# Kernel optimization log

Hardware: AMD Instinct MI355X
Metric: run time of the kernel (lower is better)

## Reference

```python
import jax, jax.numpy as jnp
import numpy as np

EPS = 1e-5

def _layernorm(x, gamma, beta, axes):
    mean = jnp.mean(x, axis=axes, keepdims=True)
    var = jnp.var(x, axis=axes, keepdims=True)
    return (x - mean) * jax.lax.rsqrt(var + EPS) * gamma + beta

def setup_inputs() -> dict:
    key = jax.random.key(0)
    ks = jax.random.split(key, 14)
    B, N1, N2, D1, D2 = 128, 32, 32, 23, 13
    E, H, F = 72, 256, 128
    N = N1 + N2
    s = 0.05
    return {
        "x_a": jax.random.normal(ks[0], (B, N1, D1), jnp.float32),
        "x_b": jax.random.normal(ks[1], (B, N2, D2), jnp.float32),
        "W_a": jax.random.normal(ks[2], (D1, E), jnp.float32) * s,
        "b_a": jnp.zeros((E,), jnp.float32),
        "W_b": jax.random.normal(ks[3], (D2, E), jnp.float32) * s,
        "b_b": jnp.zeros((E,), jnp.float32),
        "ln0_g": jnp.ones((N, E), jnp.float32),
        "ln0_b": jnp.zeros((N, E), jnp.float32),
        "W_g": jax.random.normal(ks[4], (2 * E, H), jnp.float32) * s,
        "b_g": jnp.zeros((H,), jnp.float32),
        "lng_g": jnp.ones((H,), jnp.float32),
        "lng_b": jnp.zeros((H,), jnp.float32),
        "W_f": jax.random.normal(ks[5], (H, F), jnp.float32) * s,
        "b_f": jnp.zeros((F,), jnp.float32),
    }

def reference(x_a, x_b, W_a, b_a, W_b, b_b, ln0_g, ln0_b,
              W_g, b_g, lng_g, lng_b, W_f, b_f):
    # SplitEmbedding: per-group linear embed, concat along entity dim
    a = jnp.concatenate([x_a @ W_a + b_a, x_b @ W_b + b_b], axis=-2)  # [B, N, E]
    # LayerNorm over last two dims (num_entities, embed_dim) jointly
    a = _layernorm(a, ln0_g, ln0_b, axes=(-2, -1))
    B, N, E = a.shape
    # ij(): aij[b, i, j] = concat(a[b, i], a[b, j])  -> [B, N, N, 2E]
    ai = jnp.broadcast_to(a[:, :, None, :], (B, N, N, E))
    aj = jnp.broadcast_to(a[:, None, :, :], (B, N, N, E))
    aij = jnp.concatenate([ai, aj], axis=-1)
    # g: Linear(2E, H) + ELU, then LayerNorm(H)
    g = jax.nn.elu(aij @ W_g + b_g)  # [B, N, N, H]
    g = _layernorm(g, lng_g, lng_b, axes=(-1,))
    # sum over both pairwise dims
    s = jnp.sum(g, axis=(-3, -2))  # [B, H]
    # f: Linear(H, F) + ELU
    return jax.nn.elu(s @ W_f + b_f)  # [B, F]
```

## Files before the change

### kernel.cpp

```cpp
#include <hip/hip_runtime.h>
#include <hip/hip_bf16.h>

#define EPS 1e-5f

#define OFF_ABAR 0
#define OFF_U    589824
#define OFF_V    2686976
#define OFF_PART 4784128

__device__ __forceinline__ float elu(float z) {
    return z > 0.f ? z : __expf(z) - 1.f;
}

__global__ __launch_bounds__(256) void k_embed_ln0(
    const float* __restrict__ xa, const float* __restrict__ xb,
    const float* __restrict__ Wa, const float* __restrict__ ba,
    const float* __restrict__ Wb, const float* __restrict__ bb,
    const float* __restrict__ g0, const float* __restrict__ b0,
    float* __restrict__ abar) {
    int b = blockIdx.x;
    int tid = threadIdx.x;
    float vals[18];
    float s1 = 0.f, s2 = 0.f;
    for (int m = 0; m < 18; ++m) {
        int k = tid + 256 * m;
        int e = k % 72;
        int n = k / 72;
        float acc;
        if (n < 32) {
            acc = ba[e];
            const float* x = xa + (b * 32 + n) * 23;
            #pragma unroll
            for (int d = 0; d < 23; ++d) acc = fmaf(x[d], Wa[d * 72 + e], acc);
        } else {
            acc = bb[e];
            const float* x = xb + (b * 32 + (n - 32)) * 13;
            #pragma unroll
            for (int d = 0; d < 13; ++d) acc = fmaf(x[d], Wb[d * 72 + e], acc);
        }
        vals[m] = acc;
        s1 += acc;
        s2 = fmaf(acc, acc, s2);
    }
    #pragma unroll
    for (int off = 32; off >= 1; off >>= 1) {
        s1 += __shfl_xor(s1, off, 64);
        s2 += __shfl_xor(s2, off, 64);
    }
    __shared__ float r1[4], r2[4];
    int w = tid >> 6;
    if ((tid & 63) == 0) { r1[w] = s1; r2[w] = s2; }
    __syncthreads();
    float t1 = r1[0] + r1[1] + r1[2] + r1[3];
    float t2 = r2[0] + r2[1] + r2[2] + r2[3];
    float mean = t1 * (1.f / 4608.f);
    float var  = fmaf(-mean, mean, t2 * (1.f / 4608.f));
    float rsq  = rsqrtf(var + EPS);
    float* ab = abar + b * 4608;
    for (int m = 0; m < 18; ++m) {
        int k = tid + 256 * m;
        ab[k] = fmaf((vals[m] - mean) * rsq, g0[k], b0[k]);
    }
}

__global__ __launch_bounds__(256) void k_uv(
    const float* __restrict__ abar, const float* __restrict__ Wg,
    const float* __restrict__ bg,
    float* __restrict__ U, float* __restrict__ V) {
    int blk = blockIdx.x;
    int b = blk >> 2;
    int q = blk & 3;
    int h = threadIdx.x;
    __shared__ float sa[72 * 16];
    const float* src = abar + (b * 64 + q * 16) * 72;
    for (int k = threadIdx.x; k < 72 * 16; k += 256) {
        int e = k >> 4, n = k & 15;
        sa[k] = src[n * 72 + e];
    }
    __syncthreads();
    float u[16], v[16];
    #pragma unroll
    for (int n = 0; n < 16; ++n) { u[n] = 0.f; v[n] = 0.f; }
    for (int e = 0; e < 72; ++e) {
        float wu = Wg[e * 256 + h];
        float wv = Wg[(72 + e) * 256 + h];
        const float4* sp = (const float4*)&sa[e * 16];
        #pragma unroll
        for (int n4 = 0; n4 < 4; ++n4) {
            float4 s4 = sp[n4];
            u[n4*4+0] = fmaf(s4.x, wu, u[n4*4+0]); v[n4*4+0] = fmaf(s4.x, wv, v[n4*4+0]);
            u[n4*4+1] = fmaf(s4.y, wu, u[n4*4+1]); v[n4*4+1] = fmaf(s4.y, wv, v[n4*4+1]);
            u[n4*4+2] = fmaf(s4.z, wu, u[n4*4+2]); v[n4*4+2] = fmaf(s4.z, wv, v[n4*4+2]);
            u[n4*4+3] = fmaf(s4.w, wu, u[n4*4+3]); v[n4*4+3] = fmaf(s4.w, wv, v[n4*4+3]);
        }
    }
    float bgh = bg[h];
    int base = (b * 64 + q * 16) * 256 + h;
    #pragma unroll
    for (int n = 0; n < 16; ++n) {
        U[base + n * 256] = u[n] + bgh;
        V[base + n * 256] = v[n];
    }
}

__global__ __launch_bounds__(1024, 8) void k_pair(
    const float* __restrict__ U, const float* __restrict__ V,
    float* __restrict__ part) {
    int b  = blockIdx.x >> 2;
    int pc = blockIdx.x & 3;
    int i0 = pc * 16;
    int t = threadIdx.x;
    int w = t >> 6, l = t & 63;
    __shared__ float Vs[64 * 256];
    const float* Vb = V + b * 16384;
    #pragma unroll
    for (int it = 0; it < 4; ++it) {
        int k = t * 4 + it * 4096;
        int j = k >> 8, h0 = k & 255;
        float4 val = *(const float4*)&Vb[k];
        *(float4*)&Vs[j * 256 + (h0 ^ ((j & 7) << 2))] = val;
    }
    __syncthreads();

    const float* Urow = U + (size_t)(b * 64 + i0 + w) * 256;
    int swzA = (l & 7) << 2;
    const float* VrowA = Vs + l * 256;
    float s1 = 0.f, s2 = 0.f;
    for (int c = 0; c < 64; ++c) {
        float4 u4 = *(const float4*)&Urow[c * 4];
        float4 v4 = *(const float4*)&VrowA[(c * 4) ^ swzA];
        float e0 = elu(u4.x + v4.x);
        float e1 = elu(u4.y + v4.y);
        float e2 = elu(u4.z + v4.z);
        float e3 = elu(u4.w + v4.w);
        s1 += (e0 + e1) + (e2 + e3);
        s2 = fmaf(e0, e0, fmaf(e1, e1, fmaf(e2, e2, fmaf(e3, e3, s2))));
    }
    float mu  = s1 * (1.f / 256.f);
    float var = fmaf(-mu, mu, s2 * (1.f / 256.f));
    float rsq = rsqrtf(var + EPS);
    float mr  = mu * rsq;

    float4 u4 = *(const float4*)&Urow[l * 4];
    float4 acc = make_float4(0.f, 0.f, 0.f, 0.f);
    for (int j = 0; j < 64; ++j) {
        float rj = __shfl(rsq, j, 64);
        float mj = __shfl(mr,  j, 64);
        float4 v4 = *(const float4*)&Vs[j * 256 + ((l * 4) ^ ((j & 7) << 2))];
        float e0 = elu(u4.x + v4.x);
        float e1 = elu(u4.y + v4.y);
        float e2 = elu(u4.z + v4.z);
        float e3 = elu(u4.w + v4.w);
        acc.x = fmaf(e0, rj, acc.x) - mj;
        acc.y = fmaf(e1, rj, acc.y) - mj;
        acc.z = fmaf(e2, rj, acc.z) - mj;
        acc.w = fmaf(e3, rj, acc.w) - mj;
    }

    __syncthreads();
    *(float4*)&Vs[w * 256 + l * 4] = acc;
    __syncthreads();
    if (t < 256) {
        float r = 0.f;
        #pragma unroll
        for (int ww = 0; ww < 16; ++ww) r += Vs[ww * 256 + t];
        part[(b * 4 + pc) * 256 + t] = r;
    }
}

__global__ __launch_bounds__(128) void k_out(
    const float* __restrict__ part,
    const float* __restrict__ lgg, const float* __restrict__ lgb,
    const float* __restrict__ Wf,  const float* __restrict__ bfb,
    float* __restrict__ out) {
    int b = blockIdx.x;
    int f = threadIdx.x;
    __shared__ float sh[256];
    for (int h = f; h < 256; h += 128) {
        float s = part[(b * 4 + 0) * 256 + h] + part[(b * 4 + 1) * 256 + h]
                + part[(b * 4 + 2) * 256 + h] + part[(b * 4 + 3) * 256 + h];
        sh[h] = fmaf(lgg[h], s, 4096.f * lgb[h]);
    }
    __syncthreads();
    float acc = bfb[f];
    for (int h = 0; h < 256; ++h)
        acc = fmaf(sh[h], Wf[h * 128 + f], acc);
    float r = acc > 0.f ? acc : __expf(acc) - 1.f;
    out[b * 128 + f] = r;
}

extern "C" void kernel_launch(void* const* d_in, const int* in_sizes, int n_in,
                              void* d_out, int out_size, void* d_ws, size_t ws_size,
                              hipStream_t stream) {
    const float* xa  = (const float*)d_in[0];
    const float* xb  = (const float*)d_in[1];
    const float* Wa  = (const float*)d_in[2];
    const float* ba  = (const float*)d_in[3];
    const float* Wb  = (const float*)d_in[4];
    const float* bb  = (const float*)d_in[5];
    const float* g0  = (const float*)d_in[6];
    const float* b0  = (const float*)d_in[7];
    const float* Wg  = (const float*)d_in[8];
    const float* bg  = (const float*)d_in[9];
    const float* lgg = (const float*)d_in[10];
    const float* lgb = (const float*)d_in[11];
    const float* Wf  = (const float*)d_in[12];
    const float* bfb = (const float*)d_in[13];
    float* out = (float*)d_out;

    float* ws   = (float*)d_ws;
    float* abar = ws + OFF_ABAR;
    float* U    = ws + OFF_U;
    float* V    = ws + OFF_V;
    float* part = ws + OFF_PART;

    k_embed_ln0<<<128, 256, 0, stream>>>(xa, xb, Wa, ba, Wb, bb, g0, b0, abar);
    k_uv<<<512, 256, 0, stream>>>(abar, Wg, bg, U, V);
    k_pair<<<512, 1024, 0, stream>>>(U, V, part);
    k_out<<<128, 128, 0, stream>>>(part, lgg, lgb, Wf, bfb, out);
}
```

Measured before the change: 179.2 us.

## Compute pairwise ELU once, stage as bf16 in LDS, regrid pair kernel

Restructures the pairwise kernel so each ELU value is computed once, with row LayerNorm statistics derived from that pass, and the activations are cached as packed bf16 in swizzled shared memory for the normalized accumulation pass. This removes the second ELU/exp evaluation that the old two-pass design required. The grid is split into 16 chunks per batch with 512-thread blocks, and the output kernel sums 16 partials and splits its matvec across two thread halves. The bf16 truncation of cached activations reduces accuracy of the summed features.

```diff
diff --git a/kernel.cpp b/kernel.cpp
--- a/kernel.cpp
+++ b/kernel.cpp
@@ -103,90 +103,115 @@
     }
 }
 
-__global__ __launch_bounds__(1024, 8) void k_pair(
+__global__ __launch_bounds__(512, 8) void k_pair(
     const float* __restrict__ U, const float* __restrict__ V,
     float* __restrict__ part) {
-    int b  = blockIdx.x >> 2;
-    int pc = blockIdx.x & 3;
-    int i0 = pc * 16;
+    int blk = blockIdx.x;
+    int b = blk >> 4, ic = blk & 15;
     int t = threadIdx.x;
-    int w = t >> 6, l = t & 63;
-    __shared__ float Vs[64 * 256];
-    const float* Vb = V + b * 16384;
-    #pragma unroll
-    for (int it = 0; it < 4; ++it) {
-        int k = t * 4 + it * 4096;
-        int j = k >> 8, h0 = k & 255;
-        float4 val = *(const float4*)&Vb[k];
-        *(float4*)&Vs[j * 256 + (h0 ^ ((j & 7) << 2))] = val;
-    }
-    __syncthreads();
-
-    const float* Urow = U + (size_t)(b * 64 + i0 + w) * 256;
-    int swzA = (l & 7) << 2;
-    const float* VrowA = Vs + l * 256;
-    float s1 = 0.f, s2 = 0.f;
-    for (int c = 0; c < 64; ++c) {
-        float4 u4 = *(const float4*)&Urow[c * 4];
-        float4 v4 = *(const float4*)&VrowA[(c * 4) ^ swzA];
-        float e0 = elu(u4.x + v4.x);
-        float e1 = elu(u4.y + v4.y);
-        float e2 = elu(u4.z + v4.z);
-        float e3 = elu(u4.w + v4.w);
-        s1 += (e0 + e1) + (e2 + e3);
-        s2 = fmaf(e0, e0, fmaf(e1, e1, fmaf(e2, e2, fmaf(e3, e3, s2))));
-    }
-    float mu  = s1 * (1.f / 256.f);
-    float var = fmaf(-mu, mu, s2 * (1.f / 256.f));
-    float rsq = rsqrtf(var + EPS);
-    float mr  = mu * rsq;
-
-    float4 u4 = *(const float4*)&Urow[l * 4];
-    float4 acc = make_float4(0.f, 0.f, 0.f, 0.f);
-    for (int j = 0; j < 64; ++j) {
-        float rj = __shfl(rsq, j, 64);
-        float mj = __shfl(mr,  j, 64);
-        float4 v4 = *(const float4*)&Vs[j * 256 + ((l * 4) ^ ((j & 7) << 2))];
-        float e0 = elu(u4.x + v4.x);
-        float e1 = elu(u4.y + v4.y);
-        float e2 = elu(u4.z + v4.z);
-        float e3 = elu(u4.w + v4.w);
-        acc.x = fmaf(e0, rj, acc.x) - mj;
-        acc.y = fmaf(e1, rj, acc.y) - mj;
-        acc.z = fmaf(e2, rj, acc.z) - mj;
-        acc.w = fmaf(e3, rj, acc.w) - mj;
-    }
-
-    __syncthreads();
-    *(float4*)&Vs[w * 256 + l * 4] = acc;
-    __syncthreads();
-    if (t < 256) {
-        float r = 0.f;
-        #pragma unroll
-        for (int ww = 0; ww < 16; ++ww) r += Vs[ww * 256 + t];
-        part[(b * 4 + pc) * 256 + t] = r;
-    }
-}
-
-__global__ __launch_bounds__(128) void k_out(
+    int j  = t >> 3;
+    int oc = t & 7;
+    __shared__ __align__(16) unsigned Ew[64 * 128];
+    __shared__ float rsq_s[64], mr_s[64];
+    float* sc = (float*)Ew;
+
+    const float* __restrict__ Vrow  = V + (size_t)(b * 64 + j) * 256;
+    const float* __restrict__ Ubase = U + (size_t)(b * 64) * 256;
+
+    int p4 = t & 63;
+    int jq = t >> 6;
+    float acc0 = 0.f, acc1 = 0.f, acc2 = 0.f, acc3 = 0.f;
+
+    for (int ii = 0; ii < 4; ++ii) {
+        const float* __restrict__ Urow = Ubase + (size_t)(ic * 4 + ii) * 256;
+        float s1 = 0.f, s2 = 0.f;
+        #pragma unroll
+        for (int c = 0; c < 8; ++c) {
+            int h = oc * 4 + c * 32;
+            float4 v4 = *(const float4*)&Vrow[h];
+            float4 u4 = *(const float4*)&Urow[h];
+            float e0 = elu(u4.x + v4.x);
+            float e1 = elu(u4.y + v4.y);
+            float e2 = elu(u4.z + v4.z);
+            float e3 = elu(u4.w + v4.w);
+            s1 += (e0 + e1) + (e2 + e3);
+            s2 = fmaf(e0, e0, fmaf(e1, e1, fmaf(e2, e2, fmaf(e3, e3, s2))));
+            unsigned w0 = __builtin_amdgcn_perm(__float_as_uint(e1), __float_as_uint(e0), 0x07060302u);
+            unsigned w1 = __builtin_amdgcn_perm(__float_as_uint(e3), __float_as_uint(e2), 0x07060302u);
+            int hw0  = oc * 2 + c * 16;
+            int addr = (j << 7) + (hw0 ^ (c << 1) ^ ((j & 7) << 1) ^ ((j & 1) << 4));
+            *(uint2*)&Ew[addr] = make_uint2(w0, w1);
+        }
+        #pragma unroll
+        for (int d = 1; d <= 4; d <<= 1) {
+            s1 += __shfl_xor(s1, d, 64);
+            s2 += __shfl_xor(s2, d, 64);
+        }
+        float mu  = s1 * (1.f / 256.f);
+        float var = fmaf(-mu, mu, s2 * (1.f / 256.f));
+        float rsq = rsqrtf(var + EPS);
+        if (oc == 0) { rsq_s[j] = rsq; mr_s[j] = mu * rsq; }
+        __syncthreads();
+        float mloc = 0.f;
+        #pragma unroll
+        for (int jj = 0; jj < 8; ++jj) {
+            int jb = jq * 8 + jj;
+            float r = rsq_s[jb];
+            mloc += mr_s[jb];
+            int hw = p4 * 2;
+            int addr = (jb << 7) + (hw ^ (((hw >> 4) & 7) << 1) ^ ((jb & 7) << 1) ^ ((jb & 1) << 4));
+            uint2 w = *(const uint2*)&Ew[addr];
+            float f0 = __uint_as_float(w.x << 16);
+            float f1 = __uint_as_float(w.x & 0xffff0000u);
+            float f2 = __uint_as_float(w.y << 16);
+            float f3 = __uint_as_float(w.y & 0xffff0000u);
+            acc0 = fmaf(f0, r, acc0);
+            acc1 = fmaf(f1, r, acc1);
+            acc2 = fmaf(f2, r, acc2);
+            acc3 = fmaf(f3, r, acc3);
+        }
+        acc0 -= mloc; acc1 -= mloc; acc2 -= mloc; acc3 -= mloc;
+        __syncthreads();
+    }
+    *(float4*)&sc[(jq * 64 + p4) * 4] = make_float4(acc0, acc1, acc2, acc3);
+    __syncthreads();
+    if (t < 64) {
+        float4 r = make_float4(0.f, 0.f, 0.f, 0.f);
+        #pragma unroll
+        for (int q = 0; q < 8; ++q) {
+            float4 x = *(const float4*)&sc[(q * 64 + t) * 4];
+            r.x += x.x; r.y += x.y; r.z += x.z; r.w += x.w;
+        }
+        *(float4*)&part[(size_t)blk * 256 + t * 4] = r;
+    }
+}
+
+__global__ __launch_bounds__(256) void k_out(
     const float* __restrict__ part,
     const float* __restrict__ lgg, const float* __restrict__ lgb,
     const float* __restrict__ Wf,  const float* __restrict__ bfb,
     float* __restrict__ out) {
     int b = blockIdx.x;
-    int f = threadIdx.x;
+    int t = threadIdx.x;
     __shared__ float sh[256];
-    for (int h = f; h < 256; h += 128) {
-        float s = part[(b * 4 + 0) * 256 + h] + part[(b * 4 + 1) * 256 + h]
-                + part[(b * 4 + 2) * 256 + h] + part[(b * 4 + 3) * 256 + h];
-        sh[h] = fmaf(lgg[h], s, 4096.f * lgb[h]);
-    }
-    __syncthreads();
-    float acc = bfb[f];
-    for (int h = 0; h < 256; ++h)
+    __shared__ float ps[256];
+    {
+        float s = 0.f;
+        #pragma unroll
+        for (int k = 0; k < 16; ++k) s += part[(size_t)(b * 16 + k) * 256 + t];
+        sh[t] = fmaf(lgg[t], s, 4096.f * lgb[t]);
+    }
+    __syncthreads();
+    int f = t & 127, half = t >> 7;
+    float acc = 0.f;
+    for (int h = half * 128; h < half * 128 + 128; ++h)
         acc = fmaf(sh[h], Wf[h * 128 + f], acc);
-    float r = acc > 0.f ? acc : __expf(acc) - 1.f;
-    out[b * 128 + f] = r;
+    ps[t] = acc;
+    __syncthreads();
+    if (t < 128) {
+        float r = ps[t] + ps[t + 128] + bfb[t];
+        out[b * 128 + t] = r > 0.f ? r : __expf(r) - 1.f;
+    }
 }
 
 extern "C" void kernel_launch(void* const* d_in, const int* in_sizes, int n_in,
@@ -216,6 +241,6 @@
 
     k_embed_ln0<<<128, 256, 0, stream>>>(xa, xb, Wa, ba, Wb, bb, g0, b0, abar);
     k_uv<<<512, 256, 0, stream>>>(abar, Wg, bg, U, V);
-    k_pair<<<512, 1024, 0, stream>>>(U, V, part);
-    k_out<<<128, 128, 0, stream>>>(part, lgg, lgb, Wf, bfb, out);
-}
+    k_pair<<<2048, 512, 0, stream>>>(U, V, part);
+    k_out<<<128, 256, 0, stream>>>(part, lgg, lgb, Wf, bfb, out);
+}
```

Measured after the change: 289.4 us. 61.5% more time.

## Compute pairwise ELU once per element with in-register LayerNorm stats

Applied to the files above, without the earlier changes.

Restructures the pairwise kernel so each group of 16 threads owns one j row of V in registers and loops over 32 U rows held in shared memory. The per-pair LayerNorm statistics are reduced with a 16-lane shuffle and then applied directly to the ELU values kept in registers. Previously the ELU was evaluated twice per element, once for the statistics and once for accumulation. This removes that redundant exp work at the cost of a shuffle reduction per pair and a larger register footprint. The block tiling changes to 512 threads covering 32x32 (i, j) pairs.

```diff
diff --git a/kernel.cpp b/kernel.cpp
--- a/kernel.cpp
+++ b/kernel.cpp
@@ -103,68 +103,82 @@
     }
 }
 
-__global__ __launch_bounds__(1024, 8) void k_pair(
+__global__ __launch_bounds__(512, 4) void k_pair(
     const float* __restrict__ U, const float* __restrict__ V,
     float* __restrict__ part) {
-    int b  = blockIdx.x >> 2;
-    int pc = blockIdx.x & 3;
-    int i0 = pc * 16;
-    int t = threadIdx.x;
-    int w = t >> 6, l = t & 63;
-    __shared__ float Vs[64 * 256];
-    const float* Vb = V + b * 16384;
-    #pragma unroll
-    for (int it = 0; it < 4; ++it) {
-        int k = t * 4 + it * 4096;
-        int j = k >> 8, h0 = k & 255;
-        float4 val = *(const float4*)&Vb[k];
-        *(float4*)&Vs[j * 256 + (h0 ^ ((j & 7) << 2))] = val;
-    }
-    __syncthreads();
-
-    const float* Urow = U + (size_t)(b * 64 + i0 + w) * 256;
-    int swzA = (l & 7) << 2;
-    const float* VrowA = Vs + l * 256;
-    float s1 = 0.f, s2 = 0.f;
-    for (int c = 0; c < 64; ++c) {
-        float4 u4 = *(const float4*)&Urow[c * 4];
-        float4 v4 = *(const float4*)&VrowA[(c * 4) ^ swzA];
-        float e0 = elu(u4.x + v4.x);
-        float e1 = elu(u4.y + v4.y);
-        float e2 = elu(u4.z + v4.z);
-        float e3 = elu(u4.w + v4.w);
-        s1 += (e0 + e1) + (e2 + e3);
-        s2 = fmaf(e0, e0, fmaf(e1, e1, fmaf(e2, e2, fmaf(e3, e3, s2))));
-    }
-    float mu  = s1 * (1.f / 256.f);
-    float var = fmaf(-mu, mu, s2 * (1.f / 256.f));
-    float rsq = rsqrtf(var + EPS);
-    float mr  = mu * rsq;
-
-    float4 u4 = *(const float4*)&Urow[l * 4];
-    float4 acc = make_float4(0.f, 0.f, 0.f, 0.f);
-    for (int j = 0; j < 64; ++j) {
-        float rj = __shfl(rsq, j, 64);
-        float mj = __shfl(mr,  j, 64);
-        float4 v4 = *(const float4*)&Vs[j * 256 + ((l * 4) ^ ((j & 7) << 2))];
-        float e0 = elu(u4.x + v4.x);
-        float e1 = elu(u4.y + v4.y);
-        float e2 = elu(u4.z + v4.z);
-        float e3 = elu(u4.w + v4.w);
-        acc.x = fmaf(e0, rj, acc.x) - mj;
-        acc.y = fmaf(e1, rj, acc.y) - mj;
-        acc.z = fmaf(e2, rj, acc.z) - mj;
-        acc.w = fmaf(e3, rj, acc.w) - mj;
-    }
-
-    __syncthreads();
-    *(float4*)&Vs[w * 256 + l * 4] = acc;
+    int blk = blockIdx.x;
+    int b  = blk >> 2;
+    int ih = (blk >> 1) & 1;
+    int jh = blk & 1;
+    int t  = threadIdx.x;
+    int j32 = t >> 4;
+    int hc  = t & 15;
+
+    __shared__ float Us[32 * 256];
+
+    const float* Ug = U + (size_t)(b * 64 + ih * 32) * 256;
+    #pragma unroll
+    for (int r = 0; r < 4; ++r) {
+        int k = t * 4 + r * 2048;
+        *(float4*)&Us[k] = *(const float4*)&Ug[k];
+    }
+
+    const float* Vrow = V + (size_t)(b * 64 + jh * 32 + j32) * 256;
+    float v[16];
+    #pragma unroll
+    for (int c = 0; c < 4; ++c) {
+        float4 v4 = *(const float4*)&Vrow[hc * 4 + 64 * c];
+        v[c*4+0] = v4.x; v[c*4+1] = v4.y; v[c*4+2] = v4.z; v[c*4+3] = v4.w;
+    }
+
+    __syncthreads();
+
+    float acc[16];
+    #pragma unroll
+    for (int k = 0; k < 16; ++k) acc[k] = 0.f;
+    float macc = 0.f;
+
+    for (int i = 0; i < 32; ++i) {
+        const float* ur = &Us[i * 256];
+        float e[16];
+        float s1 = 0.f, s2 = 0.f;
+        #pragma unroll
+        for (int c = 0; c < 4; ++c) {
+            float4 u4 = *(const float4*)&ur[hc * 4 + 64 * c];
+            float e0 = elu(u4.x + v[c*4+0]);
+            float e1 = elu(u4.y + v[c*4+1]);
+            float e2 = elu(u4.z + v[c*4+2]);
+            float e3 = elu(u4.w + v[c*4+3]);
+            e[c*4+0] = e0; e[c*4+1] = e1; e[c*4+2] = e2; e[c*4+3] = e3;
+            s1 += (e0 + e1) + (e2 + e3);
+            s2 = fmaf(e0, e0, fmaf(e1, e1, fmaf(e2, e2, fmaf(e3, e3, s2))));
+        }
+        #pragma unroll
+        for (int d = 1; d <= 8; d <<= 1) {
+            s1 += __shfl_xor(s1, d, 64);
+            s2 += __shfl_xor(s2, d, 64);
+        }
+        float mu  = s1 * (1.f / 256.f);
+        float var = fmaf(-mu, mu, s2 * (1.f / 256.f));
+        float rsq = rsqrtf(var + EPS);
+        macc += mu * rsq;
+        #pragma unroll
+        for (int k = 0; k < 16; ++k) acc[k] = fmaf(e[k], rsq, acc[k]);
+    }
+    #pragma unroll
+    for (int k = 0; k < 16; ++k) acc[k] -= macc;
+
+    __syncthreads();
+    #pragma unroll
+    for (int c = 0; c < 4; ++c)
+        *(float4*)&Us[j32 * 256 + hc * 4 + 64 * c] =
+            make_float4(acc[c*4+0], acc[c*4+1], acc[c*4+2], acc[c*4+3]);
     __syncthreads();
     if (t < 256) {
         float r = 0.f;
         #pragma unroll
-        for (int ww = 0; ww < 16; ++ww) r += Vs[ww * 256 + t];
-        part[(b * 4 + pc) * 256 + t] = r;
+        for (int q = 0; q < 32; ++q) r += Us[q * 256 + t];
+        part[(size_t)blk * 256 + t] = r;
     }
 }
 
@@ -216,6 +230,6 @@
 
     k_embed_ln0<<<128, 256, 0, stream>>>(xa, xb, Wa, ba, Wb, bb, g0, b0, abar);
     k_uv<<<512, 256, 0, stream>>>(abar, Wg, bg, U, V);
-    k_pair<<<512, 1024, 0, stream>>>(U, V, part);
+    k_pair<<<512, 512, 0, stream>>>(U, V, part);
     k_out<<<128, 128, 0, stream>>>(part, lgg, lgb, Wf, bfb, out);
 }
```

Result: faster. 161.3 us (-10.0%).
